# Optimization experiments

Hardware: AMD Instinct MI355X
Metric: run time of the kernel (lower is better)

The kernel has to match this reference:

```python
import jax, jax.numpy as jnp
import numpy as np

DIM = 1024
HEADS = 16
HEAD_DIM = DIM // HEADS
THETA = 10000.0


def _freqs_cis(d, n, theta=THETA):
    # complex rotary frequencies, shape (n, d//2)
    pos = jnp.arange(n, dtype=jnp.float32)
    inv = 1.0 / theta ** (jnp.arange(0, d, 2, dtype=jnp.float32) / d)
    ang = jnp.outer(pos, inv)
    return jax.lax.complex(jnp.cos(ang), jnp.sin(ang))


def _to_complex(x):
    # (..., d) -> (..., d//2) complex via adjacent pairs
    xr = x.astype(jnp.float32).reshape(*x.shape[:-1], -1, 2)
    return jax.lax.complex(xr[..., 0], xr[..., 1])


def _to_real(xc):
    # (..., d//2) complex -> (..., d) interleaved real/imag
    return jnp.stack([jnp.real(xc), jnp.imag(xc)], axis=-1).reshape(*xc.shape[:-1], -1)


def setup_inputs() -> dict:
    key = jax.random.key(0)
    k1, k2, k3 = jax.random.split(key, 3)
    b, seq = 2, 2048
    x = jax.random.normal(k1, (b, DIM, seq), dtype=jnp.float32)
    w_qkv = jax.random.normal(k2, (3 * DIM, DIM), dtype=jnp.float32) * (DIM ** -0.5)
    w_out = jax.random.normal(k3, (DIM, DIM), dtype=jnp.float32) * (DIM ** -0.5)
    return {"x": x, "w_qkv": w_qkv, "w_out": w_out}


def reference(x, w_qkv, w_out):
    b, dim, n = x.shape
    h, hd = HEADS, HEAD_DIM
    scale = hd ** -0.5
    xt = jnp.swapaxes(x, -1, -2)                      # (b, t, dim)
    qkv = jnp.einsum('btd,ed->bte', xt, w_qkv)        # (b, t, 3*dim)
    q, k, v = jnp.split(qkv, 3, axis=-1)
    q = q.reshape(b, n, h, hd)
    k = k.reshape(b, n, h, hd)
    v = v.reshape(b, n, h, hd)
    # rotary embedding on q, k
    fc = _freqs_cis(hd, n)[None, :, None, :]          # (1, t, 1, hd//2)
    q = _to_real(_to_complex(q) * fc).astype(x.dtype)
    k = _to_real(_to_complex(k) * fc).astype(x.dtype)
    # naive full attention
    logits = jnp.einsum('bqhd,bkhd->bhqk', q, k) * scale
    probs = jax.nn.softmax(logits, axis=-1)
    out = jnp.einsum('bhqk,bkhd->bqhd', probs, v)     # (b, t, h, hd)
    out = out.reshape(b, n, dim)
    out = jnp.einsum('btd,ed->bte', out, w_out)       # (b, t, dim)
    return jnp.swapaxes(out, -1, -2)                  # (b, dim, t)
```

## Files before the change

### kernel.cpp

```cpp
#include <hip/hip_runtime.h>
#include <hip/hip_bf16.h>
#include <math.h>

#define B 2
#define N 2048
#define D 1024
#define H 16
#define HD 64

typedef __attribute__((ext_vector_type(8))) short short8;
typedef __attribute__((ext_vector_type(4))) float f32x4;
typedef __attribute__((ext_vector_type(16))) float f32x16;
typedef __attribute__((ext_vector_type(4))) unsigned short ush4;
typedef __attribute__((ext_vector_type(4))) unsigned int uint4v;

__device__ __forceinline__ float bf2f(unsigned short u) {
  unsigned int x = ((unsigned int)u) << 16;
  float f;
  __builtin_memcpy(&f, &x, 4);
  return f;
}
__device__ __forceinline__ unsigned short f2bf(float f) {
  unsigned int x;
  __builtin_memcpy(&x, &f, 4);
  x = x + 0x7fffu + ((x >> 16) & 1u);
  return (unsigned short)(x >> 16);
}
__device__ __forceinline__ unsigned int pk2(float lo, float hi) {
  union { __hip_bfloat162 h; unsigned int u; } cv;
  cv.h = __float22bfloat162_rn(make_float2(lo, hi));
  return cv.u;
}
__device__ __forceinline__ short8 mk_frag(unsigned int w0, unsigned int w1,
                                          unsigned int w2, unsigned int w3) {
  union { uint4v u; short8 s; } cv;
  cv.u = (uint4v){w0, w1, w2, w3};
  return cv.s;
}

__device__ __forceinline__ void gload16(const unsigned short* g, unsigned short* l) {
  __builtin_amdgcn_global_load_lds(
      (const __attribute__((address_space(1))) unsigned int*)(const void*)g,
      (__attribute__((address_space(3))) unsigned int*)(void*)l, 16, 0, 0);
}

__global__ void conv_bf16(const float* __restrict__ src, unsigned short* __restrict__ dst, int n4) {
  int i = blockIdx.x * 256 + threadIdx.x;
  if (i >= n4) return;
  float4 v = ((const float4*)src)[i];
  ush4 o;
  o[0] = f2bf(v.x); o[1] = f2bf(v.y); o[2] = f2bf(v.z); o[3] = f2bf(v.w);
  *(ush4*)&dst[i * 4] = o;
}

__global__ __launch_bounds__(256) void transpose_x(const float* __restrict__ x,
                                                   unsigned short* __restrict__ xt) {
  __shared__ float tile[32][33];
  const int tx = threadIdx.x, ty = threadIdx.y;
  const int t0 = blockIdx.x * 32, d0 = blockIdx.y * 32, bb = blockIdx.z;
#pragma unroll
  for (int i = 0; i < 4; ++i) {
    int r = ty * 4 + i;
    tile[r][tx] = x[(size_t)bb * D * N + (size_t)(d0 + r) * N + t0 + tx];
  }
  __syncthreads();
#pragma unroll
  for (int i = 0; i < 4; ++i) {
    int r = ty * 4 + i;
    xt[((size_t)(bb * N) + t0 + r) * D + d0 + tx] = f2bf(tile[tx][r]);
  }
}

__global__ void rope_table(float2* __restrict__ tab) {
  int idx = blockIdx.x * 256 + threadIdx.x;
  int t = idx >> 5, p = idx & 31;
  float inv = powf(10000.f, -(float)p / 32.f);
  float ang = (float)t * inv;
  float s, c;
  sincosf(ang, &s, &c);
  tab[idx] = make_float2(c, s);
}

template <int MODE>
__global__ __launch_bounds__(256) void gemm_bt(const unsigned short* __restrict__ A,
                                               const unsigned short* __restrict__ Bt,
                                               float* __restrict__ outf,
                                               unsigned short* __restrict__ qkbuf,
                                               unsigned short* __restrict__ vtbuf) {
  __shared__ unsigned short Asm[128 * 64];
  __shared__ unsigned short Bsm[128 * 64];
  const int tid = threadIdx.x;
  const int lane = tid & 63, wid = tid >> 6;
  const int ln = lane & 15, lh = lane >> 4;
  const int wr = wid >> 1, wc = wid & 1;
  const int m0 = blockIdx.x * 128, n0 = blockIdx.y * 128;

  f32x4 acc[4][4];
#pragma unroll
  for (int i = 0; i < 4; ++i)
#pragma unroll
    for (int j = 0; j < 4; ++j) acc[i][j] = (f32x4){0.f, 0.f, 0.f, 0.f};

  for (int k0 = 0; k0 < 1024; k0 += 64) {
#pragma unroll
    for (int jj = 0; jj < 4; ++jj) {
      int slot = tid + jj * 256;
      int row = slot >> 3, u = slot & 7;
      int usw = (u ^ (row & 7)) * 8;
      gload16(&A[(size_t)(m0 + row) * 1024 + k0 + usw], &Asm[slot * 8]);
    }
#pragma unroll
    for (int jj = 0; jj < 4; ++jj) {
      int slot = tid + jj * 256;
      int row = slot >> 3, u = slot & 7;
      int usw = (u ^ (row & 7)) * 8;
      gload16(&Bt[(size_t)(n0 + row) * 1024 + k0 + usw], &Bsm[slot * 8]);
    }
    __syncthreads();
#pragma unroll
    for (int s = 0; s < 2; ++s) {
      short8 af[4], bfr[4];
#pragma unroll
      for (int i = 0; i < 4; ++i) {
        int row = wr * 64 + i * 16 + ln;
        int u = ((s * 4 + lh) ^ (row & 7)) * 8;
        af[i] = *(const short8*)&Asm[row * 64 + u];
      }
#pragma unroll
      for (int j = 0; j < 4; ++j) {
        int row = wc * 64 + j * 16 + ln;
        int u = ((s * 4 + lh) ^ (row & 7)) * 8;
        bfr[j] = *(const short8*)&Bsm[row * 64 + u];
      }
#pragma unroll
      for (int i = 0; i < 4; ++i)
#pragma unroll
        for (int j = 0; j < 4; ++j)
          acc[i][j] = __builtin_amdgcn_mfma_f32_16x16x32_bf16(af[i], bfr[j], acc[i][j], 0, 0, 0);
    }
    __syncthreads();
  }

#pragma unroll
  for (int i = 0; i < 4; ++i) {
    int mrow = m0 + wr * 64 + i * 16 + lh * 4;
    int bb = mrow >> 11, t = mrow & 2047;
#pragma unroll
    for (int j = 0; j < 4; ++j) {
      int e = n0 + wc * 64 + j * 16 + ln;
      if (MODE == 1) {
        float* op = outf + (size_t)bb * D * N + (size_t)e * N + t;
        *(f32x4*)op = acc[i][j];
      } else {
        if (e < 2048) {
#pragma unroll
          for (int jj = 0; jj < 4; ++jj)
            qkbuf[((size_t)(bb * N + t + jj)) * 2048 + e] = f2bf(acc[i][j][jj]);
        } else {
          ush4 v;
#pragma unroll
          for (int jj = 0; jj < 4; ++jj) v[jj] = f2bf(acc[i][j][jj]);
          *(ush4*)&vtbuf[((size_t)bb * 1024 + (e - 2048)) * N + t] = v;
        }
      }
    }
  }
}

__global__ void rope_kernel(unsigned short* __restrict__ qk, const float2* __restrict__ tab) {
  int idx = blockIdx.x * 256 + threadIdx.x;
  int e = (idx & 255) * 8;
  int t = (idx >> 8) & 2047;
  int bb = idx >> 19;
  int p0 = (e & 63) >> 1;
  const float qscl = 0.125f * 1.4426950408889634f;
  float sc = (e < 1024) ? qscl : 1.0f;
  unsigned short* p = qk + ((size_t)(bb * N + t)) * 2048 + e;
  short8 v = *(short8*)p;
#pragma unroll
  for (int q = 0; q < 4; ++q) {
    float2 cs = tab[t * 32 + p0 + q];
    float xe = bf2f((unsigned short)v[2 * q]);
    float xo = bf2f((unsigned short)v[2 * q + 1]);
    v[2 * q] = (short)f2bf((xe * cs.x - xo * cs.y) * sc);
    v[2 * q + 1] = (short)f2bf((xe * cs.y + xo * cs.x) * sc);
  }
  *(short8*)p = v;
}

__global__ __launch_bounds__(256, 2) void attn_kernel(const unsigned short* __restrict__ qk,
                                                      const unsigned short* __restrict__ vt,
                                                      unsigned short* __restrict__ ob) {
  __shared__ unsigned short Ksm[2][64 * 64];
  __shared__ unsigned short Vsm[2][64 * 64];
  const int tid = threadIdx.x;
  const int lane = tid & 63, wid = tid >> 6;
  const int l31 = lane & 31, hi = lane >> 5;
  const int L = blockIdx.x;
  const int hh = L & 31, qb = L >> 5;
  const int bb = hh >> 4, h = hh & 15;
  const unsigned short* Qg = qk + (size_t)bb * N * 2048 + h * 64;
  const unsigned short* Kg = Qg + 1024;
  const unsigned short* Vg = vt + ((size_t)bb * 1024 + h * 64) * N;

  const int q = qb * 128 + wid * 32 + l31;
  short8 qf[4];
#pragma unroll
  for (int c = 0; c < 4; ++c)
    qf[c] = *(const short8*)&Qg[(size_t)q * 2048 + c * 16 + hi * 8];

  f32x16 oL, oH;
#pragma unroll
  for (int r = 0; r < 16; ++r) { oL[r] = 0.f; oH[r] = 0.f; }
  float lrun = 0.f;

  auto STAGE = [&](int buf, int kb) {
#pragma unroll
    for (int jj = 0; jj < 2; ++jj) {
      int slot = tid + jj * 256;
      int row = slot >> 3, u = slot & 7;
      int usw = (u ^ (row & 7)) * 8;
      gload16(&Kg[(size_t)(kb + row) * 2048 + usw], &Ksm[buf][slot * 8]);
    }
#pragma unroll
    for (int jj = 0; jj < 2; ++jj) {
      int slot = tid + jj * 256;
      int row = slot >> 3, u = slot & 7;
      int usw = (u ^ (row & 7)) * 8;
      gload16(&Vg[(size_t)row * N + kb + usw], &Vsm[buf][slot * 8]);
    }
  };

  STAGE(0, 0);
  __syncthreads();
  int cur = 0;
  for (int t = 0; t < N / 64; ++t) {
    if (t < N / 64 - 1) STAGE(cur ^ 1, (t + 1) * 64);
    f32x16 s0, s1;
#pragma unroll
    for (int r = 0; r < 16; ++r) { s0[r] = 0.f; s1[r] = 0.f; }
#pragma unroll
    for (int c = 0; c < 4; ++c) {
      short8 ka = *(const short8*)&Ksm[cur][l31 * 64 + (((c * 2 + hi) ^ (l31 & 7)) * 8)];
      s0 = __builtin_amdgcn_mfma_f32_32x32x16_bf16(ka, qf[c], s0, 0, 0, 0);
      int r1 = 32 + l31;
      short8 kb2 = *(const short8*)&Ksm[cur][r1 * 64 + (((c * 2 + hi) ^ (r1 & 7)) * 8)];
      s1 = __builtin_amdgcn_mfma_f32_32x32x16_bf16(kb2, qf[c], s1, 0, 0, 0);
    }
    float lsum = 0.f;
#pragma unroll
    for (int r = 0; r < 16; ++r) {
      s0[r] = __builtin_amdgcn_exp2f(s0[r]);
      s1[r] = __builtin_amdgcn_exp2f(s1[r]);
      lsum += s0[r] + s1[r];
    }
    lrun += lsum;
    unsigned int W[16];
#pragma unroll
    for (int i = 0; i < 8; ++i) {
      W[i] = pk2(s0[2 * i], s0[2 * i + 1]);
      W[8 + i] = pk2(s1[2 * i], s1[2 * i + 1]);
    }
    short8 pf[4];
#pragma unroll
    for (int c = 0; c < 4; ++c) {
      unsigned int a0 = W[4 * c + 0], b0 = W[4 * c + 2];
      unsigned int a1 = W[4 * c + 1], b1 = W[4 * c + 3];
      asm volatile("v_permlane32_swap_b32 %0, %1" : "+v"(a0), "+v"(b0));
      asm volatile("v_permlane32_swap_b32 %0, %1" : "+v"(a1), "+v"(b1));
      pf[c] = mk_frag(a0, a1, b0, b1);
    }
#pragma unroll
    for (int c = 0; c < 4; ++c) {
      short8 va = *(const short8*)&Vsm[cur][l31 * 64 + (((c * 2 + hi) ^ (l31 & 7)) * 8)];
      oL = __builtin_amdgcn_mfma_f32_32x32x16_bf16(va, pf[c], oL, 0, 0, 0);
      int rH = 32 + l31;
      short8 vb = *(const short8*)&Vsm[cur][rH * 64 + (((c * 2 + hi) ^ (rH & 7)) * 8)];
      oH = __builtin_amdgcn_mfma_f32_32x32x16_bf16(vb, pf[c], oH, 0, 0, 0);
    }
    __syncthreads();
    cur ^= 1;
  }
  lrun += __shfl_xor(lrun, 32, 64);
  float inv = 1.f / lrun;
  unsigned short* obp = ob + ((size_t)(bb * N + q)) * 1024 + h * 64;
#pragma unroll
  for (int r4 = 0; r4 < 4; ++r4) {
    ush4 vL, vH;
#pragma unroll
    for (int i = 0; i < 4; ++i) {
      vL[i] = f2bf(oL[r4 * 4 + i] * inv);
      vH[i] = f2bf(oH[r4 * 4 + i] * inv);
    }
    *(ush4*)&obp[r4 * 8 + hi * 4] = vL;
    *(ush4*)&obp[32 + r4 * 8 + hi * 4] = vH;
  }
}

extern "C" void kernel_launch(void* const* d_in, const int* in_sizes, int n_in,
                              void* d_out, int out_size, void* d_ws, size_t ws_size,
                              hipStream_t stream) {
  const float* x = (const float*)d_in[0];
  const float* w_qkv = (const float*)d_in[1];
  const float* w_out = (const float*)d_in[2];
  float* out = (float*)d_out;
  char* ws = (char*)d_ws;

  unsigned short* wqkv_bf = (unsigned short*)ws;
  unsigned short* wout_bf = (unsigned short*)(ws + 6291456);
  unsigned short* xt      = (unsigned short*)(ws + 8388608);
  unsigned short* qkbuf   = (unsigned short*)(ws + 16777216);
  unsigned short* vtbuf   = (unsigned short*)(ws + 33554432);
  float2* tab             = (float2*)(ws + 41943040);

  conv_bf16<<<3072, 256, 0, stream>>>(w_qkv, wqkv_bf, 3072 * 1024 / 4);
  conv_bf16<<<1024, 256, 0, stream>>>(w_out, wout_bf, 1024 * 1024 / 4);
  transpose_x<<<dim3(N / 32, D / 32, B), dim3(32, 8), 0, stream>>>(x, xt);
  rope_table<<<256, 256, 0, stream>>>(tab);

  gemm_bt<0><<<dim3(32, 24), 256, 0, stream>>>(xt, wqkv_bf, nullptr, qkbuf, vtbuf);
  rope_kernel<<<4096, 256, 0, stream>>>(qkbuf, tab);
  attn_kernel<<<512, 256, 0, stream>>>(qkbuf, vtbuf, xt );
  gemm_bt<1><<<dim3(32, 8), 256, 0, stream>>>(xt, wout_bf, out, nullptr, nullptr);
}
```

Before: 132.8 us.

## Fuse RoPE into QKV GEMM epilogue and split attention keys across two warp groups

The QKV GEMM epilogue now applies the rotary embedding and the q scaling directly, using a lane shuffle to fetch the paired element. This removes the separate rope kernel and its read and write of the QK buffer. The attention kernel now uses 512 threads, with two groups of four waves, each handling half of the key range. The partial outputs and row sums are combined through shared memory at the end. s_setprio hints are also added around the MFMA sections. The cost is more LDS per block (66 KB) and an extra reduction step.

```diff
diff --git a/kernel.cpp b/kernel.cpp
--- a/kernel.cpp
+++ b/kernel.cpp
@@ -86,7 +86,8 @@
                                                const unsigned short* __restrict__ Bt,
                                                float* __restrict__ outf,
                                                unsigned short* __restrict__ qkbuf,
-                                               unsigned short* __restrict__ vtbuf) {
+                                               unsigned short* __restrict__ vtbuf,
+                                               const float2* __restrict__ tab) {
   __shared__ unsigned short Asm[128 * 64];
   __shared__ unsigned short Bsm[128 * 64];
   const int tid = threadIdx.x;
@@ -141,6 +142,7 @@
     __syncthreads();
   }
 
+  const float qscl = 0.125f * 1.4426950408889634f;
 #pragma unroll
   for (int i = 0; i < 4; ++i) {
     int mrow = m0 + wr * 64 + i * 16 + lh * 4;
@@ -153,9 +155,17 @@
         *(f32x4*)op = acc[i][j];
       } else {
         if (e < 2048) {
-#pragma unroll
-          for (int jj = 0; jj < 4; ++jj)
-            qkbuf[((size_t)(bb * N + t + jj)) * 2048 + e] = f2bf(acc[i][j][jj]);
+          float sc = (e < 1024) ? qscl : 1.0f;
+          int p0 = (e & 63) >> 1;
+          bool odd = e & 1;
+#pragma unroll
+          for (int jj = 0; jj < 4; ++jj) {
+            float a = acc[i][j][jj];
+            float pr = __shfl_xor(a, 1, 64);
+            float2 cs = tab[(t + jj) * 32 + p0];
+            float val = odd ? (pr * cs.y + a * cs.x) : (a * cs.x - pr * cs.y);
+            qkbuf[((size_t)(bb * N + t + jj)) * 2048 + e] = f2bf(val * sc);
+          }
         } else {
           ush4 v;
 #pragma unroll
@@ -167,35 +177,15 @@
   }
 }
 
-__global__ void rope_kernel(unsigned short* __restrict__ qk, const float2* __restrict__ tab) {
-  int idx = blockIdx.x * 256 + threadIdx.x;
-  int e = (idx & 255) * 8;
-  int t = (idx >> 8) & 2047;
-  int bb = idx >> 19;
-  int p0 = (e & 63) >> 1;
-  const float qscl = 0.125f * 1.4426950408889634f;
-  float sc = (e < 1024) ? qscl : 1.0f;
-  unsigned short* p = qk + ((size_t)(bb * N + t)) * 2048 + e;
-  short8 v = *(short8*)p;
-#pragma unroll
-  for (int q = 0; q < 4; ++q) {
-    float2 cs = tab[t * 32 + p0 + q];
-    float xe = bf2f((unsigned short)v[2 * q]);
-    float xo = bf2f((unsigned short)v[2 * q + 1]);
-    v[2 * q] = (short)f2bf((xe * cs.x - xo * cs.y) * sc);
-    v[2 * q + 1] = (short)f2bf((xe * cs.y + xo * cs.x) * sc);
-  }
-  *(short8*)p = v;
-}
-
-__global__ __launch_bounds__(256, 2) void attn_kernel(const unsigned short* __restrict__ qk,
+__global__ __launch_bounds__(512, 4) void attn_kernel(const unsigned short* __restrict__ qk,
                                                       const unsigned short* __restrict__ vt,
                                                       unsigned short* __restrict__ ob) {
-  __shared__ unsigned short Ksm[2][64 * 64];
-  __shared__ unsigned short Vsm[2][64 * 64];
+  __shared__ __align__(16) char smem[66048];
   const int tid = threadIdx.x;
   const int lane = tid & 63, wid = tid >> 6;
   const int l31 = lane & 31, hi = lane >> 5;
+  const int g = wid >> 2, wl = wid & 3;
+  const int tidg = tid & 255;
   const int L = blockIdx.x;
   const int hh = L & 31, qb = L >> 5;
   const int bb = hh >> 4, h = hh & 15;
@@ -203,7 +193,12 @@
   const unsigned short* Kg = Qg + 1024;
   const unsigned short* Vg = vt + ((size_t)bb * 1024 + h * 64) * N;
 
-  const int q = qb * 128 + wid * 32 + l31;
+  unsigned short* Ksm[2] = {(unsigned short*)smem + (g * 2 + 0) * 4096,
+                            (unsigned short*)smem + (g * 2 + 1) * 4096};
+  unsigned short* Vsm[2] = {(unsigned short*)(smem + 32768) + (g * 2 + 0) * 4096,
+                            (unsigned short*)(smem + 32768) + (g * 2 + 1) * 4096};
+
+  const int q = qb * 128 + wl * 32 + l31;
   short8 qf[4];
 #pragma unroll
   for (int c = 0; c < 4; ++c)
@@ -214,31 +209,33 @@
   for (int r = 0; r < 16; ++r) { oL[r] = 0.f; oH[r] = 0.f; }
   float lrun = 0.f;
 
+  const int kb0 = g * 1024;
   auto STAGE = [&](int buf, int kb) {
 #pragma unroll
     for (int jj = 0; jj < 2; ++jj) {
-      int slot = tid + jj * 256;
+      int slot = tidg + jj * 256;
       int row = slot >> 3, u = slot & 7;
       int usw = (u ^ (row & 7)) * 8;
       gload16(&Kg[(size_t)(kb + row) * 2048 + usw], &Ksm[buf][slot * 8]);
     }
 #pragma unroll
     for (int jj = 0; jj < 2; ++jj) {
-      int slot = tid + jj * 256;
+      int slot = tidg + jj * 256;
       int row = slot >> 3, u = slot & 7;
       int usw = (u ^ (row & 7)) * 8;
       gload16(&Vg[(size_t)row * N + kb + usw], &Vsm[buf][slot * 8]);
     }
   };
 
-  STAGE(0, 0);
+  STAGE(0, kb0);
   __syncthreads();
   int cur = 0;
-  for (int t = 0; t < N / 64; ++t) {
-    if (t < N / 64 - 1) STAGE(cur ^ 1, (t + 1) * 64);
+  for (int t = 0; t < 16; ++t) {
+    if (t < 15) STAGE(cur ^ 1, kb0 + (t + 1) * 64);
     f32x16 s0, s1;
 #pragma unroll
     for (int r = 0; r < 16; ++r) { s0[r] = 0.f; s1[r] = 0.f; }
+    __builtin_amdgcn_s_setprio(1);
 #pragma unroll
     for (int c = 0; c < 4; ++c) {
       short8 ka = *(const short8*)&Ksm[cur][l31 * 64 + (((c * 2 + hi) ^ (l31 & 7)) * 8)];
@@ -247,6 +244,7 @@
       short8 kb2 = *(const short8*)&Ksm[cur][r1 * 64 + (((c * 2 + hi) ^ (r1 & 7)) * 8)];
       s1 = __builtin_amdgcn_mfma_f32_32x32x16_bf16(kb2, qf[c], s1, 0, 0, 0);
     }
+    __builtin_amdgcn_s_setprio(0);
     float lsum = 0.f;
 #pragma unroll
     for (int r = 0; r < 16; ++r) {
@@ -270,6 +268,7 @@
       asm volatile("v_permlane32_swap_b32 %0, %1" : "+v"(a1), "+v"(b1));
       pf[c] = mk_frag(a0, a1, b0, b1);
     }
+    __builtin_amdgcn_s_setprio(1);
 #pragma unroll
     for (int c = 0; c < 4; ++c) {
       short8 va = *(const short8*)&Vsm[cur][l31 * 64 + (((c * 2 + hi) ^ (l31 & 7)) * 8)];
@@ -278,22 +277,56 @@
       short8 vb = *(const short8*)&Vsm[cur][rH * 64 + (((c * 2 + hi) ^ (rH & 7)) * 8)];
       oH = __builtin_amdgcn_mfma_f32_32x32x16_bf16(vb, pf[c], oH, 0, 0, 0);
     }
+    __builtin_amdgcn_s_setprio(0);
     __syncthreads();
     cur ^= 1;
   }
   lrun += __shfl_xor(lrun, 32, 64);
-  float inv = 1.f / lrun;
-  unsigned short* obp = ob + ((size_t)(bb * N + q)) * 1024 + h * 64;
-#pragma unroll
-  for (int r4 = 0; r4 < 4; ++r4) {
-    ush4 vL, vH;
-#pragma unroll
-    for (int i = 0; i < 4; ++i) {
-      vL[i] = f2bf(oL[r4 * 4 + i] * inv);
-      vH[i] = f2bf(oH[r4 * 4 + i] * inv);
-    }
-    *(ush4*)&obp[r4 * 8 + hi * 4] = vL;
-    *(ush4*)&obp[32 + r4 * 8 + hi * 4] = vH;
+
+  __syncthreads();
+  float* cmb = (float*)smem;
+  float* lbuf = (float*)(smem + 65536);
+  const int ql = wl * 32 + l31;
+  if (g) {
+#pragma unroll
+    for (int r4 = 0; r4 < 4; ++r4) {
+      int bo = (ql * 256 + r4 * 32 + hi * 16) ^ ((ql & 7) << 4);
+      *(f32x4*)((char*)cmb + bo) =
+          (f32x4){oL[r4 * 4], oL[r4 * 4 + 1], oL[r4 * 4 + 2], oL[r4 * 4 + 3]};
+      int bo2 = (ql * 256 + 128 + r4 * 32 + hi * 16) ^ ((ql & 7) << 4);
+      *(f32x4*)((char*)cmb + bo2) =
+          (f32x4){oH[r4 * 4], oH[r4 * 4 + 1], oH[r4 * 4 + 2], oH[r4 * 4 + 3]};
+    }
+    if (!hi) lbuf[ql] = lrun;
+  }
+  __syncthreads();
+  if (!g) {
+#pragma unroll
+    for (int r4 = 0; r4 < 4; ++r4) {
+      int bo = (ql * 256 + r4 * 32 + hi * 16) ^ ((ql & 7) << 4);
+      f32x4 pL = *(const f32x4*)((const char*)cmb + bo);
+      int bo2 = (ql * 256 + 128 + r4 * 32 + hi * 16) ^ ((ql & 7) << 4);
+      f32x4 pH = *(const f32x4*)((const char*)cmb + bo2);
+#pragma unroll
+      for (int i = 0; i < 4; ++i) {
+        oL[r4 * 4 + i] += pL[i];
+        oH[r4 * 4 + i] += pH[i];
+      }
+    }
+    lrun += lbuf[ql];
+    float inv = 1.f / lrun;
+    unsigned short* obp = ob + ((size_t)(bb * N + q)) * 1024 + h * 64;
+#pragma unroll
+    for (int r4 = 0; r4 < 4; ++r4) {
+      ush4 vL, vH;
+#pragma unroll
+      for (int i = 0; i < 4; ++i) {
+        vL[i] = f2bf(oL[r4 * 4 + i] * inv);
+        vH[i] = f2bf(oH[r4 * 4 + i] * inv);
+      }
+      *(ush4*)&obp[r4 * 8 + hi * 4] = vL;
+      *(ush4*)&obp[32 + r4 * 8 + hi * 4] = vH;
+    }
   }
 }
 
@@ -315,11 +348,10 @@
 
   conv_bf16<<<3072, 256, 0, stream>>>(w_qkv, wqkv_bf, 3072 * 1024 / 4);
   conv_bf16<<<1024, 256, 0, stream>>>(w_out, wout_bf, 1024 * 1024 / 4);
+  rope_table<<<256, 256, 0, stream>>>(tab);
   transpose_x<<<dim3(N / 32, D / 32, B), dim3(32, 8), 0, stream>>>(x, xt);
-  rope_table<<<256, 256, 0, stream>>>(tab);
-
-  gemm_bt<0><<<dim3(32, 24), 256, 0, stream>>>(xt, wqkv_bf, nullptr, qkbuf, vtbuf);
-  rope_kernel<<<4096, 256, 0, stream>>>(qkbuf, tab);
-  attn_kernel<<<512, 256, 0, stream>>>(qkbuf, vtbuf, xt );
-  gemm_bt<1><<<dim3(32, 8), 256, 0, stream>>>(xt, wout_bf, out, nullptr, nullptr);
-}
+
+  gemm_bt<0><<<dim3(32, 24), 256, 0, stream>>>(xt, wqkv_bf, nullptr, qkbuf, vtbuf, tab);
+  attn_kernel<<<512, 512, 0, stream>>>(qkbuf, vtbuf, xt );
+  gemm_bt<1><<<dim3(32, 8), 256, 0, stream>>>(xt, wout_bf, out, nullptr, nullptr, nullptr);
+}
```

New measurement: 140.4 us. 1.06x slower.

## Fuse prep kernels, remap GEMM blocks per XCD, raise priority around attention MFMAs

Applied to the files above, without the earlier changes.

Merges the two weight-conversion kernels and the rope-table kernel into a single launch, removing two kernel launches. Remaps GEMM block indices so that the blocks placed on one XCD share the same A rows, improving L2 reuse. Wraps the attention QK and PV MFMA sections in s_setprio so that waves issuing matrix work get scheduling priority over waves doing softmax. The remap assumes round-robin dispatch of blocks across 8 XCDs.

```diff
diff --git a/kernel.cpp b/kernel.cpp
--- a/kernel.cpp
+++ b/kernel.cpp
@@ -44,13 +44,27 @@
       (__attribute__((address_space(3))) unsigned int*)(void*)l, 16, 0, 0);
 }
 
-__global__ void conv_bf16(const float* __restrict__ src, unsigned short* __restrict__ dst, int n4) {
-  int i = blockIdx.x * 256 + threadIdx.x;
-  if (i >= n4) return;
-  float4 v = ((const float4*)src)[i];
-  ush4 o;
-  o[0] = f2bf(v.x); o[1] = f2bf(v.y); o[2] = f2bf(v.z); o[3] = f2bf(v.w);
-  *(ush4*)&dst[i * 4] = o;
+__global__ void prep_k(const float* __restrict__ wqkv, unsigned short* __restrict__ wqkv_bf,
+                       const float* __restrict__ wout, unsigned short* __restrict__ wout_bf,
+                       float2* __restrict__ tab) {
+  int blk = blockIdx.x;
+  if (blk < 4096) {
+    const float* src = (blk < 3072) ? wqkv : wout;
+    unsigned short* dst = (blk < 3072) ? wqkv_bf : wout_bf;
+    int i = (blk < 3072 ? blk : blk - 3072) * 256 + threadIdx.x;
+    float4 v = ((const float4*)src)[i];
+    ush4 o;
+    o[0] = f2bf(v.x); o[1] = f2bf(v.y); o[2] = f2bf(v.z); o[3] = f2bf(v.w);
+    *(ush4*)&dst[i * 4] = o;
+  } else {
+    int idx = (blk - 4096) * 256 + threadIdx.x;
+    int t = idx >> 5, p = idx & 31;
+    float inv = powf(10000.f, -(float)p / 32.f);
+    float ang = (float)t * inv;
+    float s, c;
+    sincosf(ang, &s, &c);
+    tab[idx] = make_float2(c, s);
+  }
 }
 
 __global__ __launch_bounds__(256) void transpose_x(const float* __restrict__ x,
@@ -69,16 +83,6 @@
     int r = ty * 4 + i;
     xt[((size_t)(bb * N) + t0 + r) * D + d0 + tx] = f2bf(tile[tx][r]);
   }
-}
-
-__global__ void rope_table(float2* __restrict__ tab) {
-  int idx = blockIdx.x * 256 + threadIdx.x;
-  int t = idx >> 5, p = idx & 31;
-  float inv = powf(10000.f, -(float)p / 32.f);
-  float ang = (float)t * inv;
-  float s, c;
-  sincosf(ang, &s, &c);
-  tab[idx] = make_float2(c, s);
 }
 
 template <int MODE>
@@ -93,13 +97,16 @@
   const int lane = tid & 63, wid = tid >> 6;
   const int ln = lane & 15, lh = lane >> 4;
   const int wr = wid >> 1, wc = wid & 1;
-  const int m0 = blockIdx.x * 128, n0 = blockIdx.y * 128;
+  const int bid = blockIdx.x;
+  const int xcd = bid & 7, j = bid >> 3;
+  const int m0 = (xcd * 4 + (j & 3)) * 128;
+  const int n0 = (j >> 2) * 128;
 
   f32x4 acc[4][4];
 #pragma unroll
   for (int i = 0; i < 4; ++i)
 #pragma unroll
-    for (int j = 0; j < 4; ++j) acc[i][j] = (f32x4){0.f, 0.f, 0.f, 0.f};
+    for (int jq = 0; jq < 4; ++jq) acc[i][jq] = (f32x4){0.f, 0.f, 0.f, 0.f};
 
   for (int k0 = 0; k0 < 1024; k0 += 64) {
 #pragma unroll
@@ -127,16 +134,16 @@
         af[i] = *(const short8*)&Asm[row * 64 + u];
       }
 #pragma unroll
-      for (int j = 0; j < 4; ++j) {
-        int row = wc * 64 + j * 16 + ln;
+      for (int jq = 0; jq < 4; ++jq) {
+        int row = wc * 64 + jq * 16 + ln;
         int u = ((s * 4 + lh) ^ (row & 7)) * 8;
-        bfr[j] = *(const short8*)&Bsm[row * 64 + u];
+        bfr[jq] = *(const short8*)&Bsm[row * 64 + u];
       }
 #pragma unroll
       for (int i = 0; i < 4; ++i)
 #pragma unroll
-        for (int j = 0; j < 4; ++j)
-          acc[i][j] = __builtin_amdgcn_mfma_f32_16x16x32_bf16(af[i], bfr[j], acc[i][j], 0, 0, 0);
+        for (int jq = 0; jq < 4; ++jq)
+          acc[i][jq] = __builtin_amdgcn_mfma_f32_16x16x32_bf16(af[i], bfr[jq], acc[i][jq], 0, 0, 0);
     }
     __syncthreads();
   }
@@ -146,20 +153,20 @@
     int mrow = m0 + wr * 64 + i * 16 + lh * 4;
     int bb = mrow >> 11, t = mrow & 2047;
 #pragma unroll
-    for (int j = 0; j < 4; ++j) {
-      int e = n0 + wc * 64 + j * 16 + ln;
+    for (int jq = 0; jq < 4; ++jq) {
+      int e = n0 + wc * 64 + jq * 16 + ln;
       if (MODE == 1) {
         float* op = outf + (size_t)bb * D * N + (size_t)e * N + t;
-        *(f32x4*)op = acc[i][j];
+        *(f32x4*)op = acc[i][jq];
       } else {
         if (e < 2048) {
 #pragma unroll
           for (int jj = 0; jj < 4; ++jj)
-            qkbuf[((size_t)(bb * N + t + jj)) * 2048 + e] = f2bf(acc[i][j][jj]);
+            qkbuf[((size_t)(bb * N + t + jj)) * 2048 + e] = f2bf(acc[i][jq][jj]);
         } else {
           ush4 v;
 #pragma unroll
-          for (int jj = 0; jj < 4; ++jj) v[jj] = f2bf(acc[i][j][jj]);
+          for (int jj = 0; jj < 4; ++jj) v[jj] = f2bf(acc[i][jq][jj]);
           *(ush4*)&vtbuf[((size_t)bb * 1024 + (e - 2048)) * N + t] = v;
         }
       }
@@ -239,6 +246,7 @@
     f32x16 s0, s1;
 #pragma unroll
     for (int r = 0; r < 16; ++r) { s0[r] = 0.f; s1[r] = 0.f; }
+    __builtin_amdgcn_s_setprio(1);
 #pragma unroll
     for (int c = 0; c < 4; ++c) {
       short8 ka = *(const short8*)&Ksm[cur][l31 * 64 + (((c * 2 + hi) ^ (l31 & 7)) * 8)];
@@ -247,6 +255,7 @@
       short8 kb2 = *(const short8*)&Ksm[cur][r1 * 64 + (((c * 2 + hi) ^ (r1 & 7)) * 8)];
       s1 = __builtin_amdgcn_mfma_f32_32x32x16_bf16(kb2, qf[c], s1, 0, 0, 0);
     }
+    __builtin_amdgcn_s_setprio(0);
     float lsum = 0.f;
 #pragma unroll
     for (int r = 0; r < 16; ++r) {
@@ -270,6 +279,7 @@
       asm volatile("v_permlane32_swap_b32 %0, %1" : "+v"(a1), "+v"(b1));
       pf[c] = mk_frag(a0, a1, b0, b1);
     }
+    __builtin_amdgcn_s_setprio(1);
 #pragma unroll
     for (int c = 0; c < 4; ++c) {
       short8 va = *(const short8*)&Vsm[cur][l31 * 64 + (((c * 2 + hi) ^ (l31 & 7)) * 8)];
@@ -278,6 +288,7 @@
       short8 vb = *(const short8*)&Vsm[cur][rH * 64 + (((c * 2 + hi) ^ (rH & 7)) * 8)];
       oH = __builtin_amdgcn_mfma_f32_32x32x16_bf16(vb, pf[c], oH, 0, 0, 0);
     }
+    __builtin_amdgcn_s_setprio(0);
     __syncthreads();
     cur ^= 1;
   }
@@ -313,13 +324,11 @@
   unsigned short* vtbuf   = (unsigned short*)(ws + 33554432);
   float2* tab             = (float2*)(ws + 41943040);
 
-  conv_bf16<<<3072, 256, 0, stream>>>(w_qkv, wqkv_bf, 3072 * 1024 / 4);
-  conv_bf16<<<1024, 256, 0, stream>>>(w_out, wout_bf, 1024 * 1024 / 4);
+  prep_k<<<4352, 256, 0, stream>>>(w_qkv, wqkv_bf, w_out, wout_bf, tab);
   transpose_x<<<dim3(N / 32, D / 32, B), dim3(32, 8), 0, stream>>>(x, xt);
-  rope_table<<<256, 256, 0, stream>>>(tab);
-
-  gemm_bt<0><<<dim3(32, 24), 256, 0, stream>>>(xt, wqkv_bf, nullptr, qkbuf, vtbuf);
+
+  gemm_bt<0><<<768, 256, 0, stream>>>(xt, wqkv_bf, nullptr, qkbuf, vtbuf);
   rope_kernel<<<4096, 256, 0, stream>>>(qkbuf, tab);
   attn_kernel<<<512, 256, 0, stream>>>(qkbuf, vtbuf, xt );
-  gemm_bt<1><<<dim3(32, 8), 256, 0, stream>>>(xt, wout_bf, out, nullptr, nullptr);
-}
+  gemm_bt<1><<<256, 256, 0, stream>>>(xt, wout_bf, out, nullptr, nullptr);
+}
```

After: 127.2 us. 1.04x faster.
